# Optimization experiments

Hardware: AMD Instinct MI355X
Metric: run time of the kernel (lower is better)

Reference implementation:

```python
import jax, jax.numpy as jnp
import numpy as np

B, S, D, H = 2, 2048, 1024, 16
HD = D // H
SCALE = HD ** -0.5
EPS = 1e-5


def setup_inputs() -> dict:
    key = jax.random.key(0)
    ks = jax.random.split(key, 12)
    s = 1.0 / np.sqrt(D)
    return {
        "query": jax.random.normal(ks[0], (B, S, D), jnp.float32),
        "key_": jax.random.normal(ks[1], (B, S, D), jnp.float32),
        "value": jax.random.normal(ks[2], (B, S, D), jnp.float32),
        "Wq": jax.random.normal(ks[3], (D, D), jnp.float32) * s,
        "bq": jnp.zeros((D,), jnp.float32),
        "Wk": jax.random.normal(ks[4], (D, D), jnp.float32) * s,
        "bk": jnp.zeros((D,), jnp.float32),
        "Wv": jax.random.normal(ks[5], (D, D), jnp.float32) * s,
        "bv": jnp.zeros((D,), jnp.float32),
        "Wo": jax.random.normal(ks[6], (D, D), jnp.float32) * s,
        "bo": jnp.zeros((D,), jnp.float32),
        "gamma": jnp.ones((D,), jnp.float32),
        "beta": jnp.zeros((D,), jnp.float32),
    }


def _split_heads(x):
    # [B,S,D] -> [B,H,S,HD]
    return x.reshape(B, S, H, HD).transpose(0, 2, 1, 3)


def reference(query, key_, value, Wq, bq, Wk, bk, Wv, bv, Wo, bo, gamma, beta):
    q = _split_heads(query @ Wq + bq)
    k = _split_heads(key_ @ Wk + bk)
    v = _split_heads(value @ Wv + bv)
    # [B,H,S,S] attention scores
    scores = jnp.einsum("bhqd,bhkd->bhqk", q, k) * SCALE
    probs = jax.nn.softmax(scores, axis=-1)  # dropout is identity in eval
    attn = jnp.einsum("bhqk,bhkd->bhqd", probs, v)
    attn = attn.transpose(0, 2, 1, 3).reshape(B, S, D)
    attn = attn @ Wo + bo
    # residual + LayerNorm
    x = query + attn
    mu = jnp.mean(x, axis=-1, keepdims=True)
    var = jnp.mean(jnp.square(x - mu), axis=-1, keepdims=True)
    out = (x - mu) * jax.lax.rsqrt(var + EPS) * gamma + beta
    return out
```

## Files before the change

### kernel.cpp

```cpp
#include <hip/hip_runtime.h>
#include <hip/hip_bf16.h>

#define DEVI __device__ __forceinline__

constexpr int Bb  = 2;
constexpr int Ss  = 2048;
constexpr int Dd  = 1024;
constexpr int Hh  = 16;
constexpr int HDh = 64;
constexpr int Mr  = Bb * Ss;
constexpr float kEps = 1e-5f;
constexpr float kQScale = 0.18033688011112043f;

typedef unsigned short u16;
typedef unsigned int   u32;
typedef u16 u16x8 __attribute__((ext_vector_type(8)));
typedef u16 u16x4 __attribute__((ext_vector_type(4)));
typedef __attribute__((ext_vector_type(8)))  short s16x8;
typedef __attribute__((ext_vector_type(16))) float f32x16;
typedef __attribute__((ext_vector_type(4)))  u32   u32x4;

DEVI float bf2f(u16 u) {
  return __builtin_bit_cast(float, ((unsigned int)u) << 16);
}
DEVI u16 f2bf(float f) {
  unsigned int x = __builtin_bit_cast(unsigned int, f);
  return (u16)((x + 0x7FFFu + ((x >> 16) & 1u)) >> 16);
}
DEVI u32 cvt_pk_bf16(float a, float b) {
  u32 r;
  asm("v_cvt_pk_bf16_f32 %0, %1, %2" : "=v"(r) : "v"(a), "v"(b));
  return r;
}
DEVI float vexp2(float x) {
  float r;
  asm("v_exp_f32 %0, %1" : "=v"(r) : "v"(x));
  return r;
}

DEVI void gload_lds16(const void* g, void* l) {
  __builtin_amdgcn_global_load_lds(
      (const __attribute__((address_space(1))) unsigned int*)(unsigned long long)(size_t)g,
      (__attribute__((address_space(3))) unsigned int*)(unsigned int)(size_t)l,
      16, 0, 0);
}


__global__ __launch_bounds__(256) void pack_a_fm(
    const float* __restrict__ X0, const float* __restrict__ X1,
    u16* __restrict__ Y0, u16* __restrict__ Y1) {
  __shared__ u16 Tl[64 * 64];
  const int t  = threadIdx.x;
  const int k0 = blockIdx.x * 64, r0 = blockIdx.y * 64;
  const float* X = blockIdx.z ? X1 : X0;
  u16*         Y = blockIdx.z ? Y1 : Y0;
#pragma unroll
  for (int i = 0; i < 4; ++i) {
    const int idx = t + i * 256;
    const int r = idx >> 4, c4 = (idx & 15) << 2;
    const float4 v = *(const float4*)(X + (size_t)(r0 + r) * 1024 + k0 + c4);
    u16x4 p;
    p[0] = f2bf(v.x); p[1] = f2bf(v.y); p[2] = f2bf(v.z); p[3] = f2bf(v.w);
    *(u16x4*)&Tl[r * 64 + (c4 ^ (8 * (r & 7)))] = p;
  }
  __syncthreads();
#pragma unroll
  for (int i = 0; i < 2; ++i) {
    const int slot = t + i * 256;
    const int f = slot >> 6, l = slot & 63;
    const int l31 = l & 31, g2 = l >> 5;
    const int r = (f >> 2) * 32 + l31;
    const int c = (f & 3) * 16 + g2 * 8;
    const u16x8 v = *(const u16x8*)&Tl[r * 64 + (c ^ (8 * (r & 7)))];
    const size_t t32 = (size_t)(r0 >> 5) + (f >> 2);
    const int s = (k0 >> 4) + (f & 3);
    *(u16x8*)(Y + (t32 * 64 + s) * 512 + l * 8) = v;
  }
}

__global__ __launch_bounds__(256) void pack_w_fm(
    const float* __restrict__ W0, const float* __restrict__ W1,
    const float* __restrict__ W2, const float* __restrict__ W3,
    u16* __restrict__ WfmBase) {
  __shared__ u16 Tl[64 * 64];
  const int t  = threadIdx.x;
  const int k0 = blockIdx.x * 64, n0 = blockIdx.y * 64;
  const int z  = blockIdx.z;
  const float* W = z == 0 ? W0 : z == 1 ? W1 : z == 2 ? W2 : W3;
  u16* out = WfmBase + (size_t)z * 1024 * 1024;
#pragma unroll
  for (int i = 0; i < 4; ++i) {
    const int idx = t + i * 256;
    const int r = idx >> 4, c4 = (idx & 15) << 2;
    const float4 v = *(const float4*)(W + (size_t)(k0 + r) * 1024 + n0 + c4);
    u16x4 p;
    p[0] = f2bf(v.x); p[1] = f2bf(v.y); p[2] = f2bf(v.z); p[3] = f2bf(v.w);
    *(u16x4*)&Tl[r * 64 + (c4 ^ (8 * (r & 7)))] = p;
  }
  __syncthreads();
#pragma unroll
  for (int i = 0; i < 2; ++i) {
    const int slot = t + i * 256;
    const int f = slot >> 6, l = slot & 63;
    const int l31 = l & 31, g2 = l >> 5;
    const int rbase = (f & 3) * 16 + g2 * 8;
    const int c = (f >> 2) * 32 + l31;
    u16x8 o;
#pragma unroll
    for (int j = 0; j < 8; ++j) {
      const int r = rbase + j;
      o[j] = Tl[r * 64 + (((c & ~3) ^ (8 * (r & 7))) | (c & 3))];
    }
    const size_t n32 = (size_t)(n0 >> 5) + (f >> 2);
    const int s = (k0 >> 4) + (f & 3);
    *(u16x8*)(out + (n32 * 64 + s) * 512 + l * 8) = o;
  }
}

template <int MODE>
__global__ __launch_bounds__(256, 2) void gemm_reg_k(
    const u16* __restrict__ A0, const u16* __restrict__ A1,
    const u16* __restrict__ Wt0, const u16* __restrict__ Wt1,
    const float* b0, const float* b1, void* C0, void* C1,
    float e0, float e1) {
  constexpr int K = 1024, N = 1024;
  const int z = blockIdx.z;
  const u16*   A    = z ? A1 : A0;
  const u16*   Wt   = z ? Wt1 : Wt0;
  const float* bias = z ? b1 : b0;
  void*        Cv   = z ? C1 : C0;
  const float  esc  = z ? e1 : e0;

  const int t = threadIdx.x;
  const int lane = t & 63, w = t >> 6;
  const int l31 = lane & 31, g2 = lane >> 5;
  const int id  = blockIdx.y * 8 + blockIdx.x;
  const int sid = (id & 7) * 32 + (id >> 3);
  const int m0 = (sid >> 3) * 128, n0 = (sid & 7) * 128;
  const int wr = w >> 1, wc = w & 1;

  const u16* a0p = A  + ((size_t)(m0 >> 5) + 2 * wr) * 32768 + lane * 8;
  const u16* a1p = a0p + 32768;
  const u16* w0p = Wt + ((size_t)(n0 >> 5) + 2 * wc) * 32768 + lane * 8;
  const u16* w1p = w0p + 32768;

  f32x16 acc00, acc01, acc10, acc11;
#pragma unroll
  for (int r = 0; r < 16; ++r) { acc00[r] = 0.f; acc01[r] = 0.f; acc10[r] = 0.f; acc11[r] = 0.f; }

  s16x8 X[8], Y[8], Z[8];
  auto loadset = [&](s16x8* R, int k0) {
    const int o = (k0 >> 4) * 512;
    R[0] = *(const s16x8*)(a0p + o);  R[1] = *(const s16x8*)(a0p + o + 512);
    R[2] = *(const s16x8*)(a1p + o);  R[3] = *(const s16x8*)(a1p + o + 512);
    R[4] = *(const s16x8*)(w0p + o);  R[5] = *(const s16x8*)(w0p + o + 512);
    R[6] = *(const s16x8*)(w1p + o);  R[7] = *(const s16x8*)(w1p + o + 512);
  };
  auto compute = [&](const s16x8* R) {
#pragma unroll
    for (int s = 0; s < 2; ++s) {
      if constexpr (MODE == 1) {
        acc00 = __builtin_amdgcn_mfma_f32_32x32x16_bf16(R[0 + s], R[4 + s], acc00, 0, 0, 0);
        acc01 = __builtin_amdgcn_mfma_f32_32x32x16_bf16(R[0 + s], R[6 + s], acc01, 0, 0, 0);
        acc10 = __builtin_amdgcn_mfma_f32_32x32x16_bf16(R[2 + s], R[4 + s], acc10, 0, 0, 0);
        acc11 = __builtin_amdgcn_mfma_f32_32x32x16_bf16(R[2 + s], R[6 + s], acc11, 0, 0, 0);
      } else {
        acc00 = __builtin_amdgcn_mfma_f32_32x32x16_bf16(R[4 + s], R[0 + s], acc00, 0, 0, 0);
        acc01 = __builtin_amdgcn_mfma_f32_32x32x16_bf16(R[4 + s], R[2 + s], acc01, 0, 0, 0);
        acc10 = __builtin_amdgcn_mfma_f32_32x32x16_bf16(R[6 + s], R[0 + s], acc10, 0, 0, 0);
        acc11 = __builtin_amdgcn_mfma_f32_32x32x16_bf16(R[6 + s], R[2 + s], acc11, 0, 0, 0);
      }
    }
  };

  loadset(X, 0); loadset(Y, 32); loadset(Z, 64);
  int k = 0;
  for (int it = 0; it < 9; ++it, k += 96) {
    compute(X); loadset(X, k + 96);
    compute(Y); loadset(Y, k + 128);
    compute(Z); loadset(Z, k + 160);
  }
  compute(X); loadset(X, 960);
  compute(Y); loadset(Y, 992);
  compute(Z);
  compute(X);
  compute(Y);

  if constexpr (MODE == 1) {
    auto storeV = [&](const f32x16& a, int i, int j) {
      const int n = n0 + (2 * wc + j) * 32 + l31;
      const float bn = bias[n];
      u16* vout = (u16*)Cv + ((size_t)(m0 >> 11)) * (1024 * 2048) + (size_t)n * 2048 +
                  (m0 & 2047) + (2 * wr + i) * 32;
#pragma unroll
      for (int c = 0; c < 4; ++c) {
        u16x4 o;
#pragma unroll
        for (int rr = 0; rr < 4; ++rr) o[rr] = f2bf(a[4 * c + rr] + bn);
        *(u16x4*)(vout + 8 * c + 4 * g2) = o;
      }
    };
    storeV(acc00, 0, 0); storeV(acc01, 0, 1); storeV(acc10, 1, 0); storeV(acc11, 1, 1);
  } else {
    auto storeNM = [&](const f32x16& a, int i, int j) {
      const int m = m0 + (2 * wr + j) * 32 + l31;
#pragma unroll
      for (int c = 0; c < 4; ++c) {
        const int nb = n0 + (2 * wc + i) * 32 + 8 * c + 4 * g2;
        const float4 b4 = *(const float4*)&bias[nb];
        if constexpr (MODE == 2) {
          float4 v;
          v.x = a[4 * c + 0] + b4.x; v.y = a[4 * c + 1] + b4.y;
          v.z = a[4 * c + 2] + b4.z; v.w = a[4 * c + 3] + b4.w;
          *(float4*)((float*)Cv + (size_t)m * N + nb) = v;
        } else {
          u16x4 o;
          o[0] = f2bf((a[4 * c + 0] + b4.x) * esc); o[1] = f2bf((a[4 * c + 1] + b4.y) * esc);
          o[2] = f2bf((a[4 * c + 2] + b4.z) * esc); o[3] = f2bf((a[4 * c + 3] + b4.w) * esc);
          *(u16x4*)((u16*)Cv + (size_t)m * N + nb) = o;
        }
      }
    };
    storeNM(acc00, 0, 0); storeNM(acc01, 0, 1); storeNM(acc10, 1, 0); storeNM(acc11, 1, 1);
  }
}

__global__ __launch_bounds__(256) void flash_mfma_k(
    const u16* __restrict__ Qb, const u16* __restrict__ Kb,
    const u16* __restrict__ Vtg, u16* __restrict__ Ofm) {
  __shared__ u16 smem[24576];
  const int t    = threadIdx.x;
  const int lane = t & 63;
  const int w    = t >> 6;
  const int l31  = lane & 31, g2 = lane >> 5;
  const int hid = (blockIdx.z * 16 + blockIdx.y) * 16 + blockIdx.x;
  const int sid = (hid & 7) * 64 + (hid >> 3);
  const int h = (sid >> 4) & 15, b = sid >> 8;
  const int q0 = (sid & 15) * 128 + w * 32;

  s16x8 qf0, qf1, qf2, qf3;
  {
    const u16* qp = Qb + ((size_t)(b * Ss + q0 + l31)) * Dd + h * HDh + 8 * g2;
    qf0 = *(const s16x8*)(qp);
    qf1 = *(const s16x8*)(qp + 16);
    qf2 = *(const s16x8*)(qp + 32);
    qf3 = *(const s16x8*)(qp + 48);
  }

  f32x16 accO0, accO1, zacc;
#pragma unroll
  for (int r = 0; r < 16; ++r) { accO0[r] = 0.f; accO1[r] = 0.f; zacc[r] = 0.f; }
  float l_run = 0.f;

  const int f0 = 2 * w, f1 = 2 * w + 1;
  const u16* kg0 = Kb + ((size_t)(b * Ss + 32 * (f0 >> 2) + l31)) * Dd + h * HDh + 16 * (f0 & 3) + 8 * g2;
  const u16* kg1 = Kb + ((size_t)(b * Ss + 32 * (f1 >> 2) + l31)) * Dd + h * HDh + 16 * (f1 & 3) + 8 * g2;
  const u16* vg0 = Vtg + ((size_t)((b * Hh + h) * HDh + 32 * (f0 >> 2) + l31)) * Ss + 16 * (f0 & 3) + 8 * g2;
  const u16* vg1 = Vtg + ((size_t)((b * Hh + h) * HDh + 32 * (f1 >> 2) + l31)) * Ss + 16 * (f1 & 3) + 8 * g2;

  auto stage = [&](int buf, int kt) {
    u16* base = &smem[buf * 8192];
    gload_lds16(kg0 + (size_t)kt * 64 * Dd, base + f0 * 512);
    gload_lds16(kg1 + (size_t)kt * 64 * Dd, base + f1 * 512);
    gload_lds16(vg0 + kt * 64, base + 4096 + f0 * 512);
    gload_lds16(vg1 + kt * 64, base + 4096 + f1 * 512);
  };

  stage(0, 0);
  stage(1, 1);

  int bi = 0;
  for (int i = 0; i < 32; ++i) {
    if (i < 31) asm volatile("s_waitcnt vmcnt(4)" ::: "memory");
    else        asm volatile("s_waitcnt vmcnt(0)" ::: "memory");
    __builtin_amdgcn_s_barrier();
    if (i + 2 < 32) {
      int sbuf = bi + 2; if (sbuf >= 3) sbuf -= 3;
      stage(sbuf, i + 2);
    }
    const u16* sb = &smem[bi * 8192];
    const int lb = lane * 8;

    f32x16 sc0, sc1;
    __builtin_amdgcn_s_setprio(1);
    {
      s16x8 ka;
      ka  = *(const s16x8*)&sb[(0 * 4 + 0) * 512 + lb];
      sc0 = __builtin_amdgcn_mfma_f32_32x32x16_bf16(ka, qf0, zacc, 0, 0, 0);
      ka  = *(const s16x8*)&sb[(0 * 4 + 1) * 512 + lb];
      sc0 = __builtin_amdgcn_mfma_f32_32x32x16_bf16(ka, qf1, sc0, 0, 0, 0);
      ka  = *(const s16x8*)&sb[(0 * 4 + 2) * 512 + lb];
      sc0 = __builtin_amdgcn_mfma_f32_32x32x16_bf16(ka, qf2, sc0, 0, 0, 0);
      ka  = *(const s16x8*)&sb[(0 * 4 + 3) * 512 + lb];
      sc0 = __builtin_amdgcn_mfma_f32_32x32x16_bf16(ka, qf3, sc0, 0, 0, 0);
    }
    __builtin_amdgcn_s_setprio(0);

    float p0[16];
    float lp = 0.f;
#pragma unroll
    for (int r = 0; r < 16; ++r) { const float e = vexp2(sc0[r]); p0[r] = e; lp += e; }
    u32 pw0[4][2];
#pragma unroll
    for (int c = 0; c < 4; ++c) {
      pw0[c][0] = cvt_pk_bf16(p0[4 * c + 0], p0[4 * c + 1]);
      pw0[c][1] = cvt_pk_bf16(p0[4 * c + 2], p0[4 * c + 3]);
    }

    __builtin_amdgcn_s_setprio(1);
    {
      s16x8 kb2;
      kb2 = *(const s16x8*)&sb[(1 * 4 + 0) * 512 + lb];
      sc1 = __builtin_amdgcn_mfma_f32_32x32x16_bf16(kb2, qf0, zacc, 0, 0, 0);
      kb2 = *(const s16x8*)&sb[(1 * 4 + 1) * 512 + lb];
      sc1 = __builtin_amdgcn_mfma_f32_32x32x16_bf16(kb2, qf1, sc1, 0, 0, 0);
      kb2 = *(const s16x8*)&sb[(1 * 4 + 2) * 512 + lb];
      sc1 = __builtin_amdgcn_mfma_f32_32x32x16_bf16(kb2, qf2, sc1, 0, 0, 0);
      kb2 = *(const s16x8*)&sb[(1 * 4 + 3) * 512 + lb];
      sc1 = __builtin_amdgcn_mfma_f32_32x32x16_bf16(kb2, qf3, sc1, 0, 0, 0);
    }
    __builtin_amdgcn_s_setprio(0);

#pragma unroll
    for (int s = 0; s < 2; ++s) {
      const int cb = 2 * (s & 1);
      u32 A0w = pw0[cb][0], B0w = pw0[cb + 1][0];
      u32 A1w = pw0[cb][1], B1w = pw0[cb + 1][1];
      asm("v_permlane32_swap_b32 %0, %1" : "+v"(A0w), "+v"(B0w));
      asm("v_permlane32_swap_b32 %0, %1" : "+v"(A1w), "+v"(B1w));
      u32x4 pv;
      pv[0] = A0w; pv[1] = A1w; pv[2] = B0w; pv[3] = B1w;
      const s16x8 pf = __builtin_bit_cast(s16x8, pv);
      const s16x8 v0 = *(const s16x8*)&sb[4096 + (0 * 4 + s) * 512 + lb];
      const s16x8 v1 = *(const s16x8*)&sb[4096 + (1 * 4 + s) * 512 + lb];
      __builtin_amdgcn_s_setprio(1);
      accO0 = __builtin_amdgcn_mfma_f32_32x32x16_bf16(v0, pf, accO0, 0, 0, 0);
      accO1 = __builtin_amdgcn_mfma_f32_32x32x16_bf16(v1, pf, accO1, 0, 0, 0);
      __builtin_amdgcn_s_setprio(0);
    }

    float p1[16];
#pragma unroll
    for (int r = 0; r < 16; ++r) { const float e = vexp2(sc1[r]); p1[r] = e; lp += e; }
    u32 pw1[4][2];
#pragma unroll
    for (int c = 0; c < 4; ++c) {
      pw1[c][0] = cvt_pk_bf16(p1[4 * c + 0], p1[4 * c + 1]);
      pw1[c][1] = cvt_pk_bf16(p1[4 * c + 2], p1[4 * c + 3]);
    }
    l_run += lp;

#pragma unroll
    for (int s = 2; s < 4; ++s) {
      const int cb = 2 * (s & 1);
      u32 A0w = pw1[cb][0], B0w = pw1[cb + 1][0];
      u32 A1w = pw1[cb][1], B1w = pw1[cb + 1][1];
      asm("v_permlane32_swap_b32 %0, %1" : "+v"(A0w), "+v"(B0w));
      asm("v_permlane32_swap_b32 %0, %1" : "+v"(A1w), "+v"(B1w));
      u32x4 pv;
      pv[0] = A0w; pv[1] = A1w; pv[2] = B0w; pv[3] = B1w;
      const s16x8 pf = __builtin_bit_cast(s16x8, pv);
      const s16x8 v0 = *(const s16x8*)&sb[4096 + (0 * 4 + s) * 512 + lb];
      const s16x8 v1 = *(const s16x8*)&sb[4096 + (1 * 4 + s) * 512 + lb];
      __builtin_amdgcn_s_setprio(1);
      accO0 = __builtin_amdgcn_mfma_f32_32x32x16_bf16(v0, pf, accO0, 0, 0, 0);
      accO1 = __builtin_amdgcn_mfma_f32_32x32x16_bf16(v1, pf, accO1, 0, 0, 0);
      __builtin_amdgcn_s_setprio(0);
    }

    bi = (bi == 2) ? 0 : bi + 1;
  }

  __syncthreads();

  const float l_tot = l_run + __shfl_xor(l_run, 32);
  const float inv = 1.f / l_tot;
  u16* Ol = &smem[w * 2304];
#pragma unroll
  for (int c = 0; c < 4; ++c) {
    u16x4 pk;
#pragma unroll
    for (int rr = 0; rr < 4; ++rr) pk[rr] = f2bf(accO0[4 * c + rr] * inv);
    *(u16x4*)&Ol[l31 * 72 + 0 * 32 + c * 8 + g2 * 4] = pk;
#pragma unroll
    for (int rr = 0; rr < 4; ++rr) pk[rr] = f2bf(accO1[4 * c + rr] * inv);
    *(u16x4*)&Ol[l31 * 72 + 1 * 32 + c * 8 + g2 * 4] = pk;
  }
  const size_t m32 = (size_t)((b * Ss + q0) >> 5);
#pragma unroll
  for (int s = 0; s < 4; ++s) {
    const u16x8 vv = *(const u16x8*)&Ol[l31 * 72 + s * 16 + g2 * 8];
    *(u16x8*)(Ofm + (m32 * 64 + h * 4 + s) * 512 + lane * 8) = vv;
  }
}

__global__ __launch_bounds__(256) void resid_ln_k(const float* __restrict__ x0,
                                                  const float* __restrict__ x1,
                                                  const float* __restrict__ gamma,
                                                  const float* __restrict__ beta,
                                                  float* __restrict__ out) {
  const int row = blockIdx.x;
  const int t   = threadIdx.x;
  const size_t base = (size_t)row * Dd + t * 4;
  const float4 a = *(const float4*)(x0 + base);
  const float4 c = *(const float4*)(x1 + base);
  float x[4] = {a.x + c.x, a.y + c.y, a.z + c.z, a.w + c.w};
  float s  = (x[0] + x[1]) + (x[2] + x[3]);
  float s2 = fmaf(x[0], x[0], fmaf(x[1], x[1], fmaf(x[2], x[2], x[3] * x[3])));
#pragma unroll
  for (int m = 1; m < 64; m <<= 1) {
    s  += __shfl_xor(s, m);
    s2 += __shfl_xor(s2, m);
  }
  __shared__ float red[8];
  const int wave = t >> 6;
  if ((t & 63) == 0) {
    red[wave]     = s;
    red[wave + 4] = s2;
  }
  __syncthreads();
  s  = (red[0] + red[1]) + (red[2] + red[3]);
  s2 = (red[4] + red[5]) + (red[6] + red[7]);
  const float mu  = s * (1.f / Dd);
  const float var = s2 * (1.f / Dd) - mu * mu;
  const float rs  = rsqrtf(var + kEps);
  const float4 g  = *(const float4*)(gamma + t * 4);
  const float4 be = *(const float4*)(beta + t * 4);
  float4 o;
  o.x = (x[0] - mu) * rs * g.x + be.x;
  o.y = (x[1] - mu) * rs * g.y + be.y;
  o.z = (x[2] - mu) * rs * g.z + be.z;
  o.w = (x[3] - mu) * rs * g.w + be.w;
  *(float4*)(out + base) = o;
}

extern "C" void kernel_launch(void* const* d_in, const int* in_sizes, int n_in,
                              void* d_out, int out_size, void* d_ws,
                              size_t ws_size, hipStream_t stream) {
  const float* query = (const float*)d_in[0];
  const float* key_  = (const float*)d_in[1];
  const float* value = (const float*)d_in[2];
  const float* Wq = (const float*)d_in[3];
  const float* bq = (const float*)d_in[4];
  const float* Wk = (const float*)d_in[5];
  const float* bk = (const float*)d_in[6];
  const float* Wv = (const float*)d_in[7];
  const float* bv = (const float*)d_in[8];
  const float* Wo = (const float*)d_in[9];
  const float* bo = (const float*)d_in[10];
  const float* gamma = (const float*)d_in[11];
  const float* beta  = (const float*)d_in[12];
  float* out = (float*)d_out;

  char* ws = (char*)d_ws;
  u16* Qb  = (u16*)(ws + (size_t)0);
  u16* Kb  = (u16*)(ws + (size_t)8 * 1024 * 1024);
  u16* Vtg = (u16*)(ws + (size_t)16 * 1024 * 1024);
  u16* WfB = (u16*)(ws + (size_t)24 * 1024 * 1024);
  u16* Wqf = WfB;
  u16* Wkf = WfB + (size_t)1 * 1024 * 1024;
  u16* Wvf = WfB + (size_t)2 * 1024 * 1024;
  u16* Wof = WfB + (size_t)3 * 1024 * 1024;
  float* Xo = (float*)(ws + (size_t)8 * 1024 * 1024);
  u16* Xv  = (u16*)d_out;
  u16* Xq  = (u16*)d_out;
  u16* Xk  = (u16*)d_out + (size_t)Mr * Dd;
  u16* Ofm = (u16*)d_out;

  pack_a_fm<<<dim3(16, 64, 1), 256, 0, stream>>>(value, value, Xv, Xv);
  pack_w_fm<<<dim3(16, 16, 4), 256, 0, stream>>>(Wq, Wk, Wv, Wo, WfB);
  gemm_reg_k<1><<<dim3(8, 32, 1), 256, 0, stream>>>(
      Xv, Xv, Wvf, Wvf, bv, bv, Vtg, Vtg, 1.f, 1.f);
  pack_a_fm<<<dim3(16, 64, 2), 256, 0, stream>>>(query, key_, Xq, Xk);
  gemm_reg_k<0><<<dim3(8, 32, 2), 256, 0, stream>>>(
      Xq, Xk, Wqf, Wkf, bq, bk, Qb, Kb, kQScale, 1.f);
  flash_mfma_k<<<dim3(16, 16, 2), 256, 0, stream>>>(Qb, Kb, Vtg, Ofm);
  gemm_reg_k<2><<<dim3(8, 32, 1), 256, 0, stream>>>(
      Ofm, Ofm, Wof, Wof, bo, bo, Xo, Xo, 1.f, 1.f);
  resid_ln_k<<<Mr, 256, 0, stream>>>(query, Xo, gamma, beta, out);
}
```

Before: 139.8 us.

## Merge all packing kernels into one launch and store output projection in bf16

The two activation-packing launches and the weight-packing launch become a single 4096-block kernel that dispatches on block index, and the workspace is remapped so Xv lives in workspace instead of the output buffer. The output-projection GEMM now writes bf16 instead of fp32, and the residual LayerNorm reads bf16, which halves that intermediate's traffic. The softmax exp loops are also interleaved with bf16 packing to drop the temporary arrays. The risks are reduced precision on the attention output before the residual add, and workspace aliasing between Xv, Qb, Kb and XoB that depends on launch order.

```diff
diff --git a/kernel.cpp b/kernel.cpp
--- a/kernel.cpp
+++ b/kernel.cpp
@@ -46,74 +46,77 @@
 }
 
 
-__global__ __launch_bounds__(256) void pack_a_fm(
+__global__ __launch_bounds__(256) void pack_all_fm(
     const float* __restrict__ X0, const float* __restrict__ X1,
-    u16* __restrict__ Y0, u16* __restrict__ Y1) {
-  __shared__ u16 Tl[64 * 64];
-  const int t  = threadIdx.x;
-  const int k0 = blockIdx.x * 64, r0 = blockIdx.y * 64;
-  const float* X = blockIdx.z ? X1 : X0;
-  u16*         Y = blockIdx.z ? Y1 : Y0;
-#pragma unroll
-  for (int i = 0; i < 4; ++i) {
-    const int idx = t + i * 256;
-    const int r = idx >> 4, c4 = (idx & 15) << 2;
-    const float4 v = *(const float4*)(X + (size_t)(r0 + r) * 1024 + k0 + c4);
-    u16x4 p;
-    p[0] = f2bf(v.x); p[1] = f2bf(v.y); p[2] = f2bf(v.z); p[3] = f2bf(v.w);
-    *(u16x4*)&Tl[r * 64 + (c4 ^ (8 * (r & 7)))] = p;
-  }
-  __syncthreads();
-#pragma unroll
-  for (int i = 0; i < 2; ++i) {
-    const int slot = t + i * 256;
-    const int f = slot >> 6, l = slot & 63;
-    const int l31 = l & 31, g2 = l >> 5;
-    const int r = (f >> 2) * 32 + l31;
-    const int c = (f & 3) * 16 + g2 * 8;
-    const u16x8 v = *(const u16x8*)&Tl[r * 64 + (c ^ (8 * (r & 7)))];
-    const size_t t32 = (size_t)(r0 >> 5) + (f >> 2);
-    const int s = (k0 >> 4) + (f & 3);
-    *(u16x8*)(Y + (t32 * 64 + s) * 512 + l * 8) = v;
-  }
-}
-
-__global__ __launch_bounds__(256) void pack_w_fm(
+    const float* __restrict__ X2,
     const float* __restrict__ W0, const float* __restrict__ W1,
     const float* __restrict__ W2, const float* __restrict__ W3,
+    u16* __restrict__ Y0, u16* __restrict__ Y1, u16* __restrict__ Y2,
     u16* __restrict__ WfmBase) {
   __shared__ u16 Tl[64 * 64];
-  const int t  = threadIdx.x;
-  const int k0 = blockIdx.x * 64, n0 = blockIdx.y * 64;
-  const int z  = blockIdx.z;
-  const float* W = z == 0 ? W0 : z == 1 ? W1 : z == 2 ? W2 : W3;
-  u16* out = WfmBase + (size_t)z * 1024 * 1024;
-#pragma unroll
-  for (int i = 0; i < 4; ++i) {
-    const int idx = t + i * 256;
-    const int r = idx >> 4, c4 = (idx & 15) << 2;
-    const float4 v = *(const float4*)(W + (size_t)(k0 + r) * 1024 + n0 + c4);
-    u16x4 p;
-    p[0] = f2bf(v.x); p[1] = f2bf(v.y); p[2] = f2bf(v.z); p[3] = f2bf(v.w);
-    *(u16x4*)&Tl[r * 64 + (c4 ^ (8 * (r & 7)))] = p;
-  }
-  __syncthreads();
-#pragma unroll
-  for (int i = 0; i < 2; ++i) {
-    const int slot = t + i * 256;
-    const int f = slot >> 6, l = slot & 63;
-    const int l31 = l & 31, g2 = l >> 5;
-    const int rbase = (f & 3) * 16 + g2 * 8;
-    const int c = (f >> 2) * 32 + l31;
-    u16x8 o;
-#pragma unroll
-    for (int j = 0; j < 8; ++j) {
-      const int r = rbase + j;
-      o[j] = Tl[r * 64 + (((c & ~3) ^ (8 * (r & 7))) | (c & 3))];
-    }
-    const size_t n32 = (size_t)(n0 >> 5) + (f >> 2);
-    const int s = (k0 >> 4) + (f & 3);
-    *(u16x8*)(out + (n32 * 64 + s) * 512 + l * 8) = o;
+  const int t   = threadIdx.x;
+  const int gid = blockIdx.x;
+  if (gid < 3072) {
+    const int z   = gid >> 10;
+    const int rem = gid & 1023;
+    const int r0  = (rem >> 4) * 64, k0 = (rem & 15) * 64;
+    const float* X = z == 0 ? X0 : z == 1 ? X1 : X2;
+    u16*         Y = z == 0 ? Y0 : z == 1 ? Y1 : Y2;
+#pragma unroll
+    for (int i = 0; i < 4; ++i) {
+      const int idx = t + i * 256;
+      const int r = idx >> 4, c4 = (idx & 15) << 2;
+      const float4 v = *(const float4*)(X + (size_t)(r0 + r) * 1024 + k0 + c4);
+      u16x4 p;
+      p[0] = f2bf(v.x); p[1] = f2bf(v.y); p[2] = f2bf(v.z); p[3] = f2bf(v.w);
+      *(u16x4*)&Tl[r * 64 + (c4 ^ (8 * (r & 7)))] = p;
+    }
+    __syncthreads();
+#pragma unroll
+    for (int i = 0; i < 2; ++i) {
+      const int slot = t + i * 256;
+      const int f = slot >> 6, l = slot & 63;
+      const int l31 = l & 31, g2 = l >> 5;
+      const int r = (f >> 2) * 32 + l31;
+      const int c = (f & 3) * 16 + g2 * 8;
+      const u16x8 v = *(const u16x8*)&Tl[r * 64 + (c ^ (8 * (r & 7)))];
+      const size_t t32 = (size_t)(r0 >> 5) + (f >> 2);
+      const int s = (k0 >> 4) + (f & 3);
+      *(u16x8*)(Y + (t32 * 64 + s) * 512 + l * 8) = v;
+    }
+  } else {
+    const int wz  = (gid - 3072) >> 8;
+    const int rem = (gid - 3072) & 255;
+    const int n0  = (rem >> 4) * 64, k0 = (rem & 15) * 64;
+    const float* W = wz == 0 ? W0 : wz == 1 ? W1 : wz == 2 ? W2 : W3;
+    u16* out = WfmBase + (size_t)wz * 1024 * 1024;
+#pragma unroll
+    for (int i = 0; i < 4; ++i) {
+      const int idx = t + i * 256;
+      const int r = idx >> 4, c4 = (idx & 15) << 2;
+      const float4 v = *(const float4*)(W + (size_t)(k0 + r) * 1024 + n0 + c4);
+      u16x4 p;
+      p[0] = f2bf(v.x); p[1] = f2bf(v.y); p[2] = f2bf(v.z); p[3] = f2bf(v.w);
+      *(u16x4*)&Tl[r * 64 + (c4 ^ (8 * (r & 7)))] = p;
+    }
+    __syncthreads();
+#pragma unroll
+    for (int i = 0; i < 2; ++i) {
+      const int slot = t + i * 256;
+      const int f = slot >> 6, l = slot & 63;
+      const int l31 = l & 31, g2 = l >> 5;
+      const int rbase = (f & 3) * 16 + g2 * 8;
+      const int c = (f >> 2) * 32 + l31;
+      u16x8 o;
+#pragma unroll
+      for (int j = 0; j < 8; ++j) {
+        const int r = rbase + j;
+        o[j] = Tl[r * 64 + (((c & ~3) ^ (8 * (r & 7))) | (c & 3))];
+      }
+      const size_t n32 = (size_t)(n0 >> 5) + (f >> 2);
+      const int s = (k0 >> 4) + (f & 3);
+      *(u16x8*)(out + (n32 * 64 + s) * 512 + l * 8) = o;
+    }
   }
 }
 
@@ -208,17 +211,10 @@
       for (int c = 0; c < 4; ++c) {
         const int nb = n0 + (2 * wc + i) * 32 + 8 * c + 4 * g2;
         const float4 b4 = *(const float4*)&bias[nb];
-        if constexpr (MODE == 2) {
-          float4 v;
-          v.x = a[4 * c + 0] + b4.x; v.y = a[4 * c + 1] + b4.y;
-          v.z = a[4 * c + 2] + b4.z; v.w = a[4 * c + 3] + b4.w;
-          *(float4*)((float*)Cv + (size_t)m * N + nb) = v;
-        } else {
-          u16x4 o;
-          o[0] = f2bf((a[4 * c + 0] + b4.x) * esc); o[1] = f2bf((a[4 * c + 1] + b4.y) * esc);
-          o[2] = f2bf((a[4 * c + 2] + b4.z) * esc); o[3] = f2bf((a[4 * c + 3] + b4.w) * esc);
-          *(u16x4*)((u16*)Cv + (size_t)m * N + nb) = o;
-        }
+        u16x4 o;
+        o[0] = f2bf((a[4 * c + 0] + b4.x) * esc); o[1] = f2bf((a[4 * c + 1] + b4.y) * esc);
+        o[2] = f2bf((a[4 * c + 2] + b4.z) * esc); o[3] = f2bf((a[4 * c + 3] + b4.w) * esc);
+        *(u16x4*)((u16*)Cv + (size_t)m * N + nb) = o;
       }
     };
     storeNM(acc00, 0, 0); storeNM(acc01, 0, 1); storeNM(acc10, 1, 0); storeNM(acc11, 1, 1);
@@ -296,15 +292,17 @@
     }
     __builtin_amdgcn_s_setprio(0);
 
-    float p0[16];
     float lp = 0.f;
-#pragma unroll
-    for (int r = 0; r < 16; ++r) { const float e = vexp2(sc0[r]); p0[r] = e; lp += e; }
     u32 pw0[4][2];
 #pragma unroll
     for (int c = 0; c < 4; ++c) {
-      pw0[c][0] = cvt_pk_bf16(p0[4 * c + 0], p0[4 * c + 1]);
-      pw0[c][1] = cvt_pk_bf16(p0[4 * c + 2], p0[4 * c + 3]);
+      const float e0 = vexp2(sc0[4 * c + 0]);
+      const float e1 = vexp2(sc0[4 * c + 1]);
+      const float e2 = vexp2(sc0[4 * c + 2]);
+      const float e3 = vexp2(sc0[4 * c + 3]);
+      lp += (e0 + e1) + (e2 + e3);
+      pw0[c][0] = cvt_pk_bf16(e0, e1);
+      pw0[c][1] = cvt_pk_bf16(e2, e3);
     }
 
     __builtin_amdgcn_s_setprio(1);
@@ -339,14 +337,16 @@
       __builtin_amdgcn_s_setprio(0);
     }
 
-    float p1[16];
-#pragma unroll
-    for (int r = 0; r < 16; ++r) { const float e = vexp2(sc1[r]); p1[r] = e; lp += e; }
     u32 pw1[4][2];
 #pragma unroll
     for (int c = 0; c < 4; ++c) {
-      pw1[c][0] = cvt_pk_bf16(p1[4 * c + 0], p1[4 * c + 1]);
-      pw1[c][1] = cvt_pk_bf16(p1[4 * c + 2], p1[4 * c + 3]);
+      const float e0 = vexp2(sc1[4 * c + 0]);
+      const float e1 = vexp2(sc1[4 * c + 1]);
+      const float e2 = vexp2(sc1[4 * c + 2]);
+      const float e3 = vexp2(sc1[4 * c + 3]);
+      lp += (e0 + e1) + (e2 + e3);
+      pw1[c][0] = cvt_pk_bf16(e0, e1);
+      pw1[c][1] = cvt_pk_bf16(e2, e3);
     }
     l_run += lp;
 
@@ -395,7 +395,7 @@
 }
 
 __global__ __launch_bounds__(256) void resid_ln_k(const float* __restrict__ x0,
-                                                  const float* __restrict__ x1,
+                                                  const u16* __restrict__ x1,
                                                   const float* __restrict__ gamma,
                                                   const float* __restrict__ beta,
                                                   float* __restrict__ out) {
@@ -403,8 +403,8 @@
   const int t   = threadIdx.x;
   const size_t base = (size_t)row * Dd + t * 4;
   const float4 a = *(const float4*)(x0 + base);
-  const float4 c = *(const float4*)(x1 + base);
-  float x[4] = {a.x + c.x, a.y + c.y, a.z + c.z, a.w + c.w};
+  const u16x4  c = *(const u16x4*)(x1 + base);
+  float x[4] = {a.x + bf2f(c[0]), a.y + bf2f(c[1]), a.z + bf2f(c[2]), a.w + bf2f(c[3])};
   float s  = (x[0] + x[1]) + (x[2] + x[3]);
   float s2 = fmaf(x[0], x[0], fmaf(x[1], x[1], fmaf(x[2], x[2], x[3] * x[3])));
 #pragma unroll
@@ -453,29 +453,28 @@
   float* out = (float*)d_out;
 
   char* ws = (char*)d_ws;
+  u16* Xv  = (u16*)(ws + (size_t)0);
   u16* Qb  = (u16*)(ws + (size_t)0);
   u16* Kb  = (u16*)(ws + (size_t)8 * 1024 * 1024);
+  u16* XoB = (u16*)(ws + (size_t)8 * 1024 * 1024);
   u16* Vtg = (u16*)(ws + (size_t)16 * 1024 * 1024);
   u16* WfB = (u16*)(ws + (size_t)24 * 1024 * 1024);
   u16* Wqf = WfB;
   u16* Wkf = WfB + (size_t)1 * 1024 * 1024;
   u16* Wvf = WfB + (size_t)2 * 1024 * 1024;
   u16* Wof = WfB + (size_t)3 * 1024 * 1024;
-  float* Xo = (float*)(ws + (size_t)8 * 1024 * 1024);
-  u16* Xv  = (u16*)d_out;
   u16* Xq  = (u16*)d_out;
   u16* Xk  = (u16*)d_out + (size_t)Mr * Dd;
   u16* Ofm = (u16*)d_out;
 
-  pack_a_fm<<<dim3(16, 64, 1), 256, 0, stream>>>(value, value, Xv, Xv);
-  pack_w_fm<<<dim3(16, 16, 4), 256, 0, stream>>>(Wq, Wk, Wv, Wo, WfB);
+  pack_all_fm<<<4096, 256, 0, stream>>>(query, key_, value, Wq, Wk, Wv, Wo,
+                                        Xq, Xk, Xv, WfB);
   gemm_reg_k<1><<<dim3(8, 32, 1), 256, 0, stream>>>(
       Xv, Xv, Wvf, Wvf, bv, bv, Vtg, Vtg, 1.f, 1.f);
-  pack_a_fm<<<dim3(16, 64, 2), 256, 0, stream>>>(query, key_, Xq, Xk);
   gemm_reg_k<0><<<dim3(8, 32, 2), 256, 0, stream>>>(
       Xq, Xk, Wqf, Wkf, bq, bk, Qb, Kb, kQScale, 1.f);
   flash_mfma_k<<<dim3(16, 16, 2), 256, 0, stream>>>(Qb, Kb, Vtg, Ofm);
-  gemm_reg_k<2><<<dim3(8, 32, 1), 256, 0, stream>>>(
-      Ofm, Ofm, Wof, Wof, bo, bo, Xo, Xo, 1.f, 1.f);
-  resid_ln_k<<<Mr, 256, 0, stream>>>(query, Xo, gamma, beta, out);
-}
+  gemm_reg_k<0><<<dim3(8, 32, 1), 256, 0, stream>>>(
+      Ofm, Ofm, Wof, Wof, bo, bo, XoB, XoB, 1.f, 1.f);
+  resid_ln_k<<<Mr, 256, 0, stream>>>(query, XoB, gamma, beta, out);
+}
```

New measurement: 134.8 us. -3.6%, faster.
